# Optimization experiments

Measured on AMD Instinct MI355X. Metric: run time of the kernel, lower is better.

The kernel has to match this reference:

```python
import jax, jax.numpy as jnp
import numpy as np

K = 5          # top_k periods
KERNEL = 25    # moving-average kernel for series decomposition
D = 64         # d_model / channels
EPS = 1e-5     # BatchNorm eps (torch default)


def setup_inputs() -> dict:
    key = jax.random.key(0)
    k0, k1, k2, k3, k4 = jax.random.split(key, 5)
    B, T = 8, 2048
    x = jax.random.normal(k0, (B, T, D), jnp.float32)
    w1 = jax.random.normal(k1, (D, D, 3, 3), jnp.float32) * 0.05
    w2 = jax.random.normal(k2, (D, D, 3, 3), jnp.float32) * 0.05
    bn1_gamma = jnp.ones((D,), jnp.float32) + 0.1 * jax.random.normal(k3, (D,), jnp.float32)
    bn2_gamma = jnp.ones((D,), jnp.float32) + 0.1 * jax.random.normal(k4, (D,), jnp.float32)
    z = jnp.zeros((D,), jnp.float32)
    o = jnp.ones((D,), jnp.float32)
    return dict(x=x, w1=w1, w2=w2,
                bn1_gamma=bn1_gamma, bn1_beta=z, bn1_mean=z, bn1_var=o,
                bn2_gamma=bn2_gamma, bn2_beta=z, bn2_mean=z, bn2_var=o)


def _moving_avg(x, kernel):
    # AvgPool1d(stride=1, padding=(kernel-1)//2, count_include_pad=False) over time.
    T = x.shape[1]
    pad = (kernel - 1) // 2
    cs = jnp.concatenate([jnp.zeros_like(x[:, :1]), jnp.cumsum(x, axis=1)], axis=1)  # [B,T+1,C]
    t = jnp.arange(T)
    lo = jnp.clip(t - pad, 0, T)          # inclusive window start
    hi = jnp.clip(t + pad + 1, 0, T)      # exclusive window end
    sums = cs[:, hi] - cs[:, lo]
    return sums / (hi - lo).astype(x.dtype)[None, :, None]


def _auto_corr(s, k):
    T = s.shape[1]
    Xf = jnp.fft.rfft(s, axis=1)
    Pm = (Xf * jnp.conj(Xf)).real.mean(axis=-1)          # [B, T//2+1]
    r = jnp.fft.irfft(Pm, n=T, axis=1)                   # [B, T]
    r = r.at[:, 0].set(-jnp.inf)                          # forbid lag 0
    vals, idx = jax.lax.top_k(r, k)                       # [B,k]
    w = jax.nn.softmax(vals, axis=1)
    return idx, w


def _bn(z, gamma, beta, mean, var):
    return (z - mean) * (gamma * jax.lax.rsqrt(var + EPS)) + beta


def _process_one(s_b, p, w1, w2, bn1, bn2):
    # s_b: [T, C]; p: scalar int period.
    # Equivalent to: roll(s_b, -p), reflect-pad time to cyc*p, fold to [C,cyc,p],
    # Conv2dResBlock (3x3 zero-pad convs + eval BN + GELU + residual), unfold, crop to T.
    T, C = s_b.shape
    U = 2 * T - 2                               # static bound: cyc*p <= T+p-1 <= 2T-2
    u = jnp.arange(U)
    cyc = (T + p - 1) // p
    v = jnp.where(u < T, u, 2 * T - 2 - u)      # reflect extension index
    g = s_b[(v + p) % T]                         # [U,C] rolled-by-(-p) then reflect-padded
    r = u // p                                   # grid row (cycle)
    c = u % p                                    # grid col (phase)

    def conv3x3(z, w):
        # zero-padded 3x3 conv on the [cyc, p] grid, expressed on the flat time axis
        out = jnp.zeros_like(z)
        for dr in (-1, 0, 1):
            for dc in (-1, 0, 1):
                valid = (r + dr >= 0) & (r + dr < cyc) & (c + dc >= 0) & (c + dc < p)
                un = jnp.clip(u + dr * p + dc, 0, U - 1)
                zn = jnp.where(valid[:, None], z[un], 0.0)    # [U,C]
                out = out + zn @ w[:, :, dr + 1, dc + 1].T    # [U,Cout]
        return out

    h = _bn(conv3x3(g, w1), *bn1)
    h = jax.nn.gelu(h, approximate=False)
    h = _bn(conv3x3(h, w2), *bn2)
    return (g + h)[:T]                           # residual + unfold-crop


def reference(x, w1, w2, bn1_gamma, bn1_beta, bn1_mean, bn1_var,
              bn2_gamma, bn2_beta, bn2_mean, bn2_var):
    trend = _moving_avg(x, KERNEL)
    s = x - trend                                # seasonal
    idx, w = _auto_corr(s, K)                    # [B,K] periods, weights
    bn1 = (bn1_gamma, bn1_beta, bn1_mean, bn1_var)
    bn2 = (bn2_gamma, bn2_beta, bn2_mean, bn2_var)
    f = lambda sb, p: _process_one(sb, p, w1, w2, bn1, bn2)
    y = jax.vmap(lambda sb, pb: jax.vmap(lambda p: f(sb, p))(pb))(s, idx)  # [B,K,T,C]
    agg = jnp.einsum('bk,bktc->btc', w, y)
    return agg + trend + x
```

## Files before the change

### kernel.cpp

```cpp
#include <hip/hip_runtime.h>
#include <hip/hip_bf16.h>
#include <math.h>

#define TB 8
#define TT 2048
#define TD 64
#define TK 5
#define TPAD 12
#define EPSBN 1e-5f
#define UMAX 4096

#define ROWS 64
#define BAND 66
#define LROWS 198

#define ROWS2 16
#define BAND2 18
#define LROWS2 54
#define SH8   432
#define BUFB  6912

#define RSTR 272

typedef __attribute__((ext_vector_type(8))) short short8;
typedef __attribute__((ext_vector_type(4))) float f32x4;

#define OFF_S     0
#define OFF_SBF   1048576
#define OFF_R     1572864
#define OFF_IDX   1581056
#define OFF_W     1581096
#define OFF_WT1   1581136
#define OFF_WT2   1599568
#define OFF_H1    1618000

__global__ __launch_bounds__(256) void k_trend(const float* __restrict__ x,
                                               float* __restrict__ out, float* __restrict__ s,
                                               __hip_bfloat16* __restrict__ sbf,
                                               const float* __restrict__ w1, const float* __restrict__ w2,
                                               __hip_bfloat16* __restrict__ wt1, __hip_bfloat16* __restrict__ wt2,
                                               float* __restrict__ r)
{
    if (blockIdx.x >= 256) {
        int d = (blockIdx.x - 256) * 256 + threadIdx.x;
        if (d < TB * 1024) r[d] = 0.f;
        if (d < 36864) {
            int j = d & 7, l = (d >> 3) & 63, nt = (d >> 9) & 3, kb = d >> 11;
            int tap = kb >> 1, half = kb & 1;
            int co = nt * 16 + (l & 15);
            int ci = half * 32 + (l >> 4) * 8 + j;
            int src = (co * 64 + ci) * 9 + tap;
            wt1[d] = __float2bfloat16(w1[src]);
            wt2[d] = __float2bfloat16(w2[src]);
        }
        return;
    }
    int gid = blockIdx.x * 256 + threadIdx.x;
    int c = gid & 63;
    int tblk = (gid >> 6) & 127;
    int b = gid >> 13;
    int t0 = tblk * 16;
    const float* base = x + (size_t)b * TT * TD + c;
    float sum = 0.f;
    for (int tt = t0 - TPAD; tt <= t0 + TPAD; ++tt)
        if (tt >= 0 && tt < TT) sum += base[(size_t)tt * TD];
    size_t o = (size_t)b * TT * TD + (size_t)t0 * TD + c;
    #pragma unroll
    for (int i = 0; i < 16; ++i) {
        int t = t0 + i;
        int lo = t - TPAD; if (lo < 0) lo = 0;
        int hi = t + TPAD; if (hi > TT - 1) hi = TT - 1;
        float tr = sum / (float)(hi - lo + 1);
        float xv = base[(size_t)t * TD];
        out[o] = xv + tr;
        float sv = xv - tr;
        s[o] = sv;
        sbf[o] = __float2bfloat16(sv);
        int addt = t + TPAD + 1, subt = t - TPAD;
        if (addt < TT) sum += base[(size_t)addt * TD];
        if (subt >= 0) sum -= base[(size_t)subt * TD];
        o += TD;
    }
}

__global__ __launch_bounds__(256) void k_autocorr(const float* __restrict__ s, float* __restrict__ r)
{
    int id = blockIdx.x;
    int b = id & 7;
    int i0 = id >> 3;
    int l0 = (i0 & 63) * 16 + 1;
    int tq = i0 >> 6;
    const float* sb = s + (size_t)b * TT * TD;
    int cg = (threadIdx.x & 15) * 4;
    int tg = threadIdx.x >> 4;
    int t0 = tq * 512 + tg * 32;
    const int RB = TD * 4;
    const int TTB = TT * TD * 4;
    float acc[16];
    #pragma unroll
    for (int j = 0; j < 16; ++j) acc[j] = 0.f;
    float4 win[16];
    int wi = t0 + l0; if (wi >= TT) wi -= TT;
    int woff = wi * RB + cg * 4;
    int aoff = t0 * RB + cg * 4;
    #pragma unroll
    for (int m = 0; m < 16; ++m) {
        win[m] = *(const float4*)((const char*)sb + woff);
        woff += RB; if (woff >= TTB) woff -= TTB;
    }
    float4 a_pf = *(const float4*)((const char*)sb + aoff);
    aoff += RB;
    for (int it = 0; it < 2; ++it) {
        #pragma unroll
        for (int jj = 0; jj < 16; ++jj) {
            float4 a = a_pf;
            a_pf = *(const float4*)((const char*)sb + aoff);
            aoff += RB;
            #pragma unroll
            for (int j = 0; j < 16; ++j) {
                float4 w = win[(jj + j) & 15];
                acc[j] = fmaf(a.x, w.x, acc[j]);
                acc[j] = fmaf(a.y, w.y, acc[j]);
                acc[j] = fmaf(a.z, w.z, acc[j]);
                acc[j] = fmaf(a.w, w.w, acc[j]);
            }
            win[jj] = *(const float4*)((const char*)sb + woff);
            woff += RB; if (woff >= TTB) woff -= TTB;
        }
    }
    __shared__ float red[16 * RSTR];
    #pragma unroll
    for (int j = 0; j < 16; ++j) red[j * RSTR + threadIdx.x] = acc[j];
    __syncthreads();
    int j = threadIdx.x >> 4, i = threadIdx.x & 15;
    float v = 0.f;
    #pragma unroll
    for (int m = 0; m < 16; ++m) v += red[j * RSTR + i + 16 * m];
    #pragma unroll
    for (int mask = 8; mask; mask >>= 1) v += __shfl_xor(v, mask);
    if (i == 0) atomicAdd(&r[(size_t)b * 1024 + (l0 - 1 + j)], v * (1.0f / 64.0f));
}

__global__ __launch_bounds__(256) void k_topk(const float* __restrict__ r,
                                              int* __restrict__ selidx, float* __restrict__ selw)
{
    int b = blockIdx.x;
    __shared__ float v[1024];
    __shared__ float redv[256]; __shared__ int redi[256];
    __shared__ int s_idx[6]; __shared__ float s_val[6]; __shared__ int slots;
    for (int i = threadIdx.x; i < 1024; i += 256) v[i] = r[(size_t)b * 1024 + i];
    if (threadIdx.x == 0) slots = 0;
    __syncthreads();
    for (int round = 0; round < 5; ++round) {
        if (slots >= 5) break;
        float bv = -INFINITY; int bi = 1 << 30;
        for (int i = threadIdx.x; i < 1024; i += 256) {
            float val = v[i];
            if (val > bv) { bv = val; bi = i; }
        }
        redv[threadIdx.x] = bv; redi[threadIdx.x] = bi;
        __syncthreads();
        for (int off = 128; off; off >>= 1) {
            if (threadIdx.x < off) {
                float ov = redv[threadIdx.x + off]; int oi = redi[threadIdx.x + off];
                float mv = redv[threadIdx.x];       int mi = redi[threadIdx.x];
                if (ov > mv || (ov == mv && oi < mi)) { redv[threadIdx.x] = ov; redi[threadIdx.x] = oi; }
            }
            __syncthreads();
        }
        if (threadIdx.x == 0) {
            int lag = redi[0] + 1; float val = redv[0];
            s_idx[slots] = lag; s_val[slots] = val; slots++;
            if (slots < 5 && lag < 1024) { s_idx[slots] = 2048 - lag; s_val[slots] = val; slots++; }
            v[lag - 1] = -INFINITY;
        }
        __syncthreads();
    }
    if (threadIdx.x == 0) {
        float mx = -INFINITY;
        for (int i = 0; i < 5; ++i) mx = fmaxf(mx, s_val[i]);
        float e[5], sum = 0.f;
        for (int i = 0; i < 5; ++i) { e[i] = expf(s_val[i] - mx); sum += e[i]; }
        for (int i = 0; i < 5; ++i) { selidx[b * TK + i] = s_idx[i]; selw[b * TK + i] = e[i] / sum; }
    }
}

__global__ __launch_bounds__(256) void k_mm1(
    const short* __restrict__ s_bf, const short* __restrict__ wtp,
    const float* __restrict__ g1, const float* __restrict__ b1,
    const float* __restrict__ m1, const float* __restrict__ v1,
    const int* __restrict__ sel, __hip_bfloat16* __restrict__ h1)
{
    int b = blockIdx.z, k = blockIdx.y;
    int p = sel[b * TK + k];
    int cyc = (TT + p - 1) / p;
    int U = cyc * p;
    int u0 = blockIdx.x * ROWS;
    if (u0 >= U) return;
    __shared__ short As[LROWS * 64];

    const short* sb = s_bf + (size_t)b * TT * TD;
    for (int q = threadIdx.x; q < LROWS * 8; q += 256) {
        int row = q >> 3, ch = (q & 7) * 8;
        int band = row / BAND, i = row - band * BAND;
        int w = u0 + (band - 1) * p - 1 + i;
        int wc = min(max(w, 0), 2 * TT - 2);
        int v = (wc < TT) ? wc : (2 * TT - 2 - wc);
        int sr = (v + p) & (TT - 1);
        short8 d = *(const short8*)(sb + (size_t)sr * TD + ch);
        int off = (row * 128 + ch * 2) ^ ((row & 7) << 4);
        *(short8*)((char*)As + off) = d;
    }
    __syncthreads();

    int lane = threadIdx.x & 63;
    int wv = threadIdx.x >> 6;
    int lr = lane & 15;
    int kg = lane >> 4;
    int lu = wv * 16 + lr;
    int u = u0 + lu;
    bool inU = (u < U);
    int r = u / p, c = u - r * p;
    bool topf = (r == 0), botf = (r == cyc - 1), leftf = (c == 0), rightf = (c == p - 1);

    f32x4 acc[4] = {};
    short8 zero = {};
    #pragma unroll
    for (int kb = 0; kb < 18; ++kb) {
        const int tap = kb >> 1, half = kb & 1;
        const int dr = tap / 3 - 1, dc = tap % 3 - 1;
        int ldsrow = (dr + 1) * BAND + lu + 1 + dc;
        int off = (ldsrow * 128 + half * 64 + kg * 16) ^ ((ldsrow & 7) << 4);
        short8 a = *(const short8*)((const char*)As + off);
        bool valid = inU
                   && !(dr == -1 && topf) && !(dr == 1 && botf)
                   && !(dc == -1 && leftf) && !(dc == 1 && rightf);
        if (!valid) a = zero;
        #pragma unroll
        for (int nt = 0; nt < 4; ++nt) {
            short8 bq = *(const short8*)(wtp + (size_t)(kb * 4 + nt) * 512 + lane * 8);
            acc[nt] = __builtin_amdgcn_mfma_f32_16x16x32_bf16(a, bq, acc[nt], 0, 0, 0);
        }
    }
    __hip_bfloat16* ho = h1 + (size_t)(b * TK + k) * (UMAX * TD);
    #pragma unroll
    for (int nt = 0; nt < 4; ++nt) {
        int co = nt * 16 + lr;
        float scale = g1[co] * rsqrtf(v1[co] + EPSBN);
        float bias = b1[co] - m1[co] * scale;
        #pragma unroll
        for (int q = 0; q < 4; ++q) {
            int uo = u0 + wv * 16 + kg * 4 + q;
            if (uo < U) {
                float z = acc[nt][q] * scale + bias;
                float ge = 0.5f * z * (1.0f + erff(z * 0.70710678118654752f));
                ho[(size_t)uo * TD + co] = __float2bfloat16(ge);
            }
        }
    }
}

__global__ __launch_bounds__(256) void k_mm2f(
    const short* __restrict__ h1, const short* __restrict__ wtp,
    const float* __restrict__ s,
    const float* __restrict__ g2, const float* __restrict__ b2,
    const float* __restrict__ m2, const float* __restrict__ v2,
    const int* __restrict__ sel, const float* __restrict__ selw,
    float* __restrict__ out)
{
    int b = blockIdx.y;
    int u0 = blockIdx.x * ROWS2;
    int tid = threadIdx.x;
    __shared__ short As[2 * LROWS2 * 64];

    int lane = tid & 63, wv = tid >> 6, lr = lane & 15, kg = lane >> 4;
    int u = u0 + lr;
    const float* sb = s + (size_t)b * TT * TD;

    f32x4 accT = {};
    float gacc[4] = {0.f, 0.f, 0.f, 0.f};
    short8 sreg[2];
    short8 zero = {};

    {
        int p0 = sel[b * TK];
        const short* hb = h1 + (size_t)(b * TK) * (UMAX * TD);
        #pragma unroll
        for (int it = 0; it < 2; ++it) {
            int q = tid + it * 256;
            if (q < SH8) {
                int row = q >> 3, ch = (q & 7) * 8;
                int band = row / BAND2, i = row - band * BAND2;
                int w = u0 + (band - 1) * p0 - 1 + i;
                int wc = min(max(w, 0), UMAX - 1);
                short8 d = *(const short8*)(hb + (size_t)wc * TD + ch);
                int off = (row * 128 + ch * 2) ^ ((row & 7) << 4);
                *(short8*)((char*)As + off) = d;
            }
        }
    }
    __syncthreads();

    for (int k = 0; k < TK; ++k) {
        int p = sel[b * TK + k];
        float wk = selw[b * TK + k];
        int cyc = (TT + p - 1) / p;
        if (k < TK - 1) {
            int pn = sel[b * TK + k + 1];
            const short* hb = h1 + (size_t)(b * TK + k + 1) * (UMAX * TD);
            #pragma unroll
            for (int it = 0; it < 2; ++it) {
                int q = tid + it * 256;
                if (q < SH8) {
                    int row = q >> 3, ch = (q & 7) * 8;
                    int band = row / BAND2, i = row - band * BAND2;
                    int w = u0 + (band - 1) * pn - 1 + i;
                    int wc = min(max(w, 0), UMAX - 1);
                    sreg[it] = *(const short8*)(hb + (size_t)wc * TD + ch);
                }
            }
        }
        const char* Ab = (const char*)As + (k & 1) * BUFB;
        int r = u / p, c = u - r * p;
        bool topf = (r == 0), botf = (r == cyc - 1), leftf = (c == 0), rightf = (c == p - 1);
        f32x4 accP[2] = {};
        #pragma unroll
        for (int kb = 0; kb < 18; ++kb) {
            const int tap = kb >> 1, half = kb & 1;
            const int dr = tap / 3 - 1, dc = tap % 3 - 1;
            int ldsrow = (dr + 1) * BAND2 + lr + 1 + dc;
            int off = (ldsrow * 128 + half * 64 + kg * 16) ^ ((ldsrow & 7) << 4);
            short8 a = *(const short8*)(Ab + off);
            bool valid = !(dr == -1 && topf) && !(dr == 1 && botf)
                       && !(dc == -1 && leftf) && !(dc == 1 && rightf);
            if (!valid) a = zero;
            short8 bq = *(const short8*)(wtp + (size_t)(kb * 4 + wv) * 512 + lane * 8);
            accP[kb & 1] = __builtin_amdgcn_mfma_f32_16x16x32_bf16(a, bq, accP[kb & 1], 0, 0, 0);
        }
        #pragma unroll
        for (int e = 0; e < 4; ++e) accT[e] += wk * (accP[0][e] + accP[1][e]);
        #pragma unroll
        for (int q = 0; q < 4; ++q) {
            int uo = u0 + kg * 4 + q;
            int sr = (uo + p) & (TT - 1);
            gacc[q] = fmaf(wk, sb[(size_t)sr * TD + wv * 16 + lr], gacc[q]);
        }
        __syncthreads();
        if (k < TK - 1) {
            char* Aw = (char*)As + ((k + 1) & 1) * BUFB;
            #pragma unroll
            for (int it = 0; it < 2; ++it) {
                int q = tid + it * 256;
                if (q < SH8) {
                    int row = q >> 3, ch = (q & 7) * 8;
                    int off = (row * 128 + ch * 2) ^ ((row & 7) << 4);
                    *(short8*)(Aw + off) = sreg[it];
                }
            }
            __syncthreads();
        }
    }

    float* ob = out + (size_t)b * TT * TD;
    int co = wv * 16 + lr;
    float scale = g2[co] * rsqrtf(v2[co] + EPSBN);
    float bias = b2[co] - m2[co] * scale;
    #pragma unroll
    for (int q = 0; q < 4; ++q) {
        int uo = u0 + kg * 4 + q;
        size_t idx = (size_t)uo * TD + co;
        ob[idx] = ob[idx] + gacc[q] + scale * accT[q] + bias;
    }
}

extern "C" void kernel_launch(void* const* d_in, const int* in_sizes, int n_in,
                              void* d_out, int out_size, void* d_ws, size_t ws_size,
                              hipStream_t stream)
{
    const float* x  = (const float*)d_in[0];
    const float* w1 = (const float*)d_in[1];
    const float* w2 = (const float*)d_in[2];
    const float* g1 = (const float*)d_in[3];
    const float* b1 = (const float*)d_in[4];
    const float* m1 = (const float*)d_in[5];
    const float* v1 = (const float*)d_in[6];
    const float* g2 = (const float*)d_in[7];
    const float* b2 = (const float*)d_in[8];
    const float* m2 = (const float*)d_in[9];
    const float* v2 = (const float*)d_in[10];

    float* ws    = (float*)d_ws;
    float* s     = ws + OFF_S;
    __hip_bfloat16* sbf = (__hip_bfloat16*)(ws + OFF_SBF);
    float* r     = ws + OFF_R;
    int*   sel   = (int*)(ws + OFF_IDX);
    float* selw  = ws + OFF_W;
    __hip_bfloat16* wt1 = (__hip_bfloat16*)(ws + OFF_WT1);
    __hip_bfloat16* wt2 = (__hip_bfloat16*)(ws + OFF_WT2);
    __hip_bfloat16* h1  = (__hip_bfloat16*)(ws + OFF_H1);
    float* out   = (float*)d_out;

    k_trend   <<<dim3(400),         dim3(256), 0, stream>>>(x, out, s, sbf, w1, w2, wt1, wt2, r);
    k_autocorr<<<dim3(2048),        dim3(256), 0, stream>>>(s, r);
    k_topk    <<<dim3(TB),          dim3(256), 0, stream>>>(r, sel, selw);
    k_mm1     <<<dim3(64, TK, TB),  dim3(256), 0, stream>>>((const short*)sbf, (const short*)wt1,
                                                            g1, b1, m1, v1, sel, h1);
    k_mm2f    <<<dim3(128, TB),     dim3(256), 0, stream>>>((const short*)h1, (const short*)wt2, s,
                                                            g2, b2, m2, v2, sel, selw, out);
}
```

Baseline: 122.1 us.

## Stage autocorrelation tiles in LDS with 64x64 time-lag blocking

```diff
diff --git a/kernel.cpp b/kernel.cpp
--- a/kernel.cpp
+++ b/kernel.cpp
@@ -19,8 +19,6 @@
 #define LROWS2 54
 #define SH8   432
 #define BUFB  6912
-
-#define RSTR 272
 
 typedef __attribute__((ext_vector_type(8))) short short8;
 typedef __attribute__((ext_vector_type(4))) float f32x4;
@@ -88,57 +86,64 @@
     int id = blockIdx.x;
     int b = id & 7;
     int i0 = id >> 3;
-    int l0 = (i0 & 63) * 16 + 1;
-    int tq = i0 >> 6;
+    int tchunk = i0 & 31;
+    int lagblk = i0 >> 5;
+    int t0 = tchunk * 64;
+    int l0 = lagblk * 64 + 1;
     const float* sb = s + (size_t)b * TT * TD;
+    __shared__ float A[64 * 64];
+    __shared__ float W[127 * 64];
+
+    #pragma unroll
+    for (int it = 0; it < 4; ++it) {
+        int q = threadIdx.x + it * 256;
+        int row = q >> 4, f4 = (q & 15) * 4;
+        *(float4*)(A + row * 64 + f4) = *(const float4*)(sb + (size_t)(t0 + row) * TD + f4);
+    }
+    for (int q = threadIdx.x; q < 127 * 16; q += 256) {
+        int row = q >> 4, f4 = (q & 15) * 4;
+        int gr = t0 + l0 + row; if (gr >= TT) gr -= TT;
+        *(float4*)(W + row * 64 + f4) = *(const float4*)(sb + (size_t)gr * TD + f4);
+    }
+    __syncthreads();
+
     int cg = (threadIdx.x & 15) * 4;
-    int tg = threadIdx.x >> 4;
-    int t0 = tq * 512 + tg * 32;
-    const int RB = TD * 4;
-    const int TTB = TT * TD * 4;
+    int slot = threadIdx.x >> 4;
+    int lsub = slot >> 2;
+    int ts = slot & 3;
+    int abase = ts * 16;
+    int wbase = ts * 16 + lsub * 16;
+
     float acc[16];
     #pragma unroll
     for (int j = 0; j < 16; ++j) acc[j] = 0.f;
     float4 win[16];
-    int wi = t0 + l0; if (wi >= TT) wi -= TT;
-    int woff = wi * RB + cg * 4;
-    int aoff = t0 * RB + cg * 4;
-    #pragma unroll
-    for (int m = 0; m < 16; ++m) {
-        win[m] = *(const float4*)((const char*)sb + woff);
-        woff += RB; if (woff >= TTB) woff -= TTB;
-    }
-    float4 a_pf = *(const float4*)((const char*)sb + aoff);
-    aoff += RB;
-    for (int it = 0; it < 2; ++it) {
-        #pragma unroll
-        for (int jj = 0; jj < 16; ++jj) {
-            float4 a = a_pf;
-            a_pf = *(const float4*)((const char*)sb + aoff);
-            aoff += RB;
-            #pragma unroll
-            for (int j = 0; j < 16; ++j) {
-                float4 w = win[(jj + j) & 15];
-                acc[j] = fmaf(a.x, w.x, acc[j]);
-                acc[j] = fmaf(a.y, w.y, acc[j]);
-                acc[j] = fmaf(a.z, w.z, acc[j]);
-                acc[j] = fmaf(a.w, w.w, acc[j]);
-            }
-            win[jj] = *(const float4*)((const char*)sb + woff);
-            woff += RB; if (woff >= TTB) woff -= TTB;
-        }
-    }
-    __shared__ float red[16 * RSTR];
-    #pragma unroll
-    for (int j = 0; j < 16; ++j) red[j * RSTR + threadIdx.x] = acc[j];
-    __syncthreads();
-    int j = threadIdx.x >> 4, i = threadIdx.x & 15;
-    float v = 0.f;
-    #pragma unroll
-    for (int m = 0; m < 16; ++m) v += red[j * RSTR + i + 16 * m];
-    #pragma unroll
-    for (int mask = 8; mask; mask >>= 1) v += __shfl_xor(v, mask);
-    if (i == 0) atomicAdd(&r[(size_t)b * 1024 + (l0 - 1 + j)], v * (1.0f / 64.0f));
+    #pragma unroll
+    for (int m = 0; m < 16; ++m) win[m] = *(const float4*)(W + (wbase + m) * 64 + cg);
+
+    #pragma unroll
+    for (int step = 0; step < 16; ++step) {
+        float4 a = *(const float4*)(A + (abase + step) * 64 + cg);
+        #pragma unroll
+        for (int j = 0; j < 16; ++j) {
+            float4 w = win[(step + j) & 15];
+            acc[j] = fmaf(a.x, w.x, acc[j]);
+            acc[j] = fmaf(a.y, w.y, acc[j]);
+            acc[j] = fmaf(a.z, w.z, acc[j]);
+            acc[j] = fmaf(a.w, w.w, acc[j]);
+        }
+        if (step < 15) win[step & 15] = *(const float4*)(W + (wbase + step + 16) * 64 + cg);
+    }
+
+    int lane = threadIdx.x & 63;
+    #pragma unroll
+    for (int j = 0; j < 16; ++j) {
+        float v = acc[j];
+        #pragma unroll
+        for (int mask = 32; mask; mask >>= 1) v += __shfl_xor(v, mask);
+        if (lane == 0)
+            atomicAdd(&r[(size_t)b * 1024 + (l0 - 1 + lsub * 16 + j)], v * (1.0f / 64.0f));
+    }
 }
 
 __global__ __launch_bounds__(256) void k_topk(const float* __restrict__ r,
@@ -401,7 +406,7 @@
     float* out   = (float*)d_out;
 
     k_trend   <<<dim3(400),         dim3(256), 0, stream>>>(x, out, s, sbf, w1, w2, wt1, wt2, r);
-    k_autocorr<<<dim3(2048),        dim3(256), 0, stream>>>(s, r);
+    k_autocorr<<<dim3(4096),        dim3(256), 0, stream>>>(s, r);
     k_topk    <<<dim3(TB),          dim3(256), 0, stream>>>(r, sel, selw);
     k_mm1     <<<dim3(64, TK, TB),  dim3(256), 0, stream>>>((const short*)sbf, (const short*)wt1,
                                                             g1, b1, m1, v1, sel, h1);
```

Result: slower. 219.4 us (+79.8%).

## Compute autocorrelation with bf16 MFMA and rescore top candidates in fp32

Applied to the files above, without the earlier changes.

```diff
diff --git a/kernel.cpp b/kernel.cpp
--- a/kernel.cpp
+++ b/kernel.cpp
@@ -20,7 +20,7 @@
 #define SH8   432
 #define BUFB  6912
 
-#define RSTR 272
+#define ACG 17
 
 typedef __attribute__((ext_vector_type(8))) short short8;
 typedef __attribute__((ext_vector_type(4))) float f32x4;
@@ -33,6 +33,7 @@
 #define OFF_WT1   1581136
 #define OFF_WT2   1599568
 #define OFF_H1    1618000
+#define OFF_CAND  6860880
 
 __global__ __launch_bounds__(256) void k_trend(const float* __restrict__ x,
                                                float* __restrict__ out, float* __restrict__ s,
@@ -83,76 +84,91 @@
     }
 }
 
-__global__ __launch_bounds__(256) void k_autocorr(const float* __restrict__ s, float* __restrict__ r)
+__global__ __launch_bounds__(256) void k_ac_mfma(const short* __restrict__ sbf16, float* __restrict__ r)
 {
     int id = blockIdx.x;
     int b = id & 7;
-    int i0 = id >> 3;
-    int l0 = (i0 & 63) * 16 + 1;
-    int tq = i0 >> 6;
-    const float* sb = s + (size_t)b * TT * TD;
-    int cg = (threadIdx.x & 15) * 4;
-    int tg = threadIdx.x >> 4;
-    int t0 = tq * 512 + tg * 32;
-    const int RB = TD * 4;
-    const int TTB = TT * TD * 4;
-    float acc[16];
-    #pragma unroll
-    for (int j = 0; j < 16; ++j) acc[j] = 0.f;
-    float4 win[16];
-    int wi = t0 + l0; if (wi >= TT) wi -= TT;
-    int woff = wi * RB + cg * 4;
-    int aoff = t0 * RB + cg * 4;
-    #pragma unroll
-    for (int m = 0; m < 16; ++m) {
-        win[m] = *(const float4*)((const char*)sb + woff);
-        woff += RB; if (woff >= TTB) woff -= TTB;
-    }
-    float4 a_pf = *(const float4*)((const char*)sb + aoff);
-    aoff += RB;
-    for (int it = 0; it < 2; ++it) {
-        #pragma unroll
-        for (int jj = 0; jj < 16; ++jj) {
-            float4 a = a_pf;
-            a_pf = *(const float4*)((const char*)sb + aoff);
-            aoff += RB;
-            #pragma unroll
-            for (int j = 0; j < 16; ++j) {
-                float4 w = win[(jj + j) & 15];
-                acc[j] = fmaf(a.x, w.x, acc[j]);
-                acc[j] = fmaf(a.y, w.y, acc[j]);
-                acc[j] = fmaf(a.z, w.z, acc[j]);
-                acc[j] = fmaf(a.w, w.w, acc[j]);
-            }
-            win[jj] = *(const float4*)((const char*)sb + woff);
-            woff += RB; if (woff >= TTB) woff -= TTB;
-        }
-    }
-    __shared__ float red[16 * RSTR];
-    #pragma unroll
-    for (int j = 0; j < 16; ++j) red[j * RSTR + threadIdx.x] = acc[j];
-    __syncthreads();
-    int j = threadIdx.x >> 4, i = threadIdx.x & 15;
-    float v = 0.f;
-    #pragma unroll
-    for (int m = 0; m < 16; ++m) v += red[j * RSTR + i + 16 * m];
-    #pragma unroll
-    for (int mask = 8; mask; mask >>= 1) v += __shfl_xor(v, mask);
-    if (i == 0) atomicAdd(&r[(size_t)b * 1024 + (l0 - 1 + j)], v * (1.0f / 64.0f));
-}
-
-__global__ __launch_bounds__(256) void k_topk(const float* __restrict__ r,
-                                              int* __restrict__ selidx, float* __restrict__ selw)
+    int slot = id >> 3;
+    int g = slot % ACG;
+    int qq = slot / ACG;
+    int d0 = g * 4;
+    int t0 = qq * 32;
+    const short* sb = sbf16 + (size_t)b * TT * TD;
+
+    __shared__ short Atile[2][1024];
+    __shared__ short Btile[6][1024];
+    __shared__ float scr[4][16 * 17];
+
+    int tid = threadIdx.x;
+    if (tid < 128) {
+        int dst = (tid * 16) ^ (((tid >> 3) & 7) << 4);
+        *(short8*)((char*)Atile[t0 & 1] + dst) =
+            *(const short8*)(sb + (size_t)((t0 & 127) * 1024) + tid * 8);
+        #pragma unroll
+        for (int j = 0; j < 4; ++j) {
+            int xi = t0 + d0 + j;
+            *(short8*)((char*)Btile[xi % 6] + dst) =
+                *(const short8*)(sb + (size_t)((xi & 127) * 1024) + tid * 8);
+        }
+    }
+    __syncthreads();
+
+    int lane = tid & 63, wv = tid >> 6;
+    int fr = lane & 15, kg = lane >> 4;
+    int roff0 = (fr * 128 + kg * 16) ^ ((fr & 7) << 4);
+    int roff1 = roff0 ^ 64;
+    int myD = d0 + wv;
+
+    f32x4 acc = {};
+    for (int stp = 0; stp < 32; ++stp) {
+        int ti = t0 + stp;
+        short8 sA, sB;
+        if (tid < 128) {
+            sA = *(const short8*)(sb + (size_t)(((ti + 1) & 127) * 1024) + tid * 8);
+            sB = *(const short8*)(sb + (size_t)(((ti + d0 + 4) & 127) * 1024) + tid * 8);
+        }
+        const char* Ab = (const char*)Atile[ti & 1];
+        const char* Bb = (const char*)Btile[(ti + myD) % 6];
+        short8 a0 = *(const short8*)(Ab + roff0);
+        short8 a1 = *(const short8*)(Ab + roff1);
+        short8 b0 = *(const short8*)(Bb + roff0);
+        short8 b1 = *(const short8*)(Bb + roff1);
+        acc = __builtin_amdgcn_mfma_f32_16x16x32_bf16(a0, b0, acc, 0, 0, 0);
+        acc = __builtin_amdgcn_mfma_f32_16x16x32_bf16(a1, b1, acc, 0, 0, 0);
+        if (tid < 128) {
+            int dst = (tid * 16) ^ (((tid >> 3) & 7) << 4);
+            *(short8*)((char*)Atile[(ti + 1) & 1] + dst) = sA;
+            *(short8*)((char*)Btile[(ti + d0 + 4) % 6] + dst) = sB;
+        }
+        __syncthreads();
+    }
+
+    float* sc = scr[wv];
+    #pragma unroll
+    for (int q = 0; q < 4; ++q)
+        sc[(kg * 4 + q) * 17 + fr] = acc[q];
+    __syncthreads();
+    if (lane < 31) {
+        int d = lane - 15;
+        int lag = 16 * myD + d;
+        if (lag >= 1 && lag <= 1024) {
+            int m0 = d < 0 ? -d : 0;
+            int m1 = d < 0 ? 16 : 16 - d;
+            float v = 0.f;
+            for (int m = m0; m < m1; ++m) v += sc[m * 17 + m + d];
+            atomicAdd(&r[(size_t)b * 1024 + (lag - 1)], v * (1.0f / 64.0f));
+        }
+    }
+}
+
+__global__ __launch_bounds__(256) void k_cand(const float* __restrict__ r, int* __restrict__ cand)
 {
     int b = blockIdx.x;
     __shared__ float v[1024];
     __shared__ float redv[256]; __shared__ int redi[256];
-    __shared__ int s_idx[6]; __shared__ float s_val[6]; __shared__ int slots;
     for (int i = threadIdx.x; i < 1024; i += 256) v[i] = r[(size_t)b * 1024 + i];
-    if (threadIdx.x == 0) slots = 0;
-    __syncthreads();
-    for (int round = 0; round < 5; ++round) {
-        if (slots >= 5) break;
+    __syncthreads();
+    for (int round = 0; round < 8; ++round) {
         float bv = -INFINITY; int bi = 1 << 30;
         for (int i = threadIdx.x; i < 1024; i += 256) {
             float val = v[i];
@@ -169,14 +185,52 @@
             __syncthreads();
         }
         if (threadIdx.x == 0) {
-            int lag = redi[0] + 1; float val = redv[0];
-            s_idx[slots] = lag; s_val[slots] = val; slots++;
-            if (slots < 5 && lag < 1024) { s_idx[slots] = 2048 - lag; s_val[slots] = val; slots++; }
+            int lag = redi[0] + 1;
+            cand[b * 8 + round] = lag;
             v[lag - 1] = -INFINITY;
         }
         __syncthreads();
     }
+}
+
+__global__ __launch_bounds__(512) void k_rescore5(const float* __restrict__ s, const int* __restrict__ cand,
+                                                  int* __restrict__ selidx, float* __restrict__ selw)
+{
+    int b = blockIdx.x;
+    int wv = threadIdx.x >> 6, lane = threadIdx.x & 63;
+    const float* sb = s + (size_t)b * TT * TD;
+    int lag = cand[b * 8 + wv];
+    int cg = (lane & 15) * 4;
+    int t0 = (lane >> 4) * 512;
+    float acc = 0.f;
+    #pragma unroll 8
+    for (int t = t0; t < t0 + 512; ++t) {
+        const float4 a = *(const float4*)(sb + ((size_t)t << 6) + cg);
+        const float4 w = *(const float4*)(sb + ((size_t)((t + lag) & (TT - 1)) << 6) + cg);
+        acc = fmaf(a.x, w.x, acc);
+        acc = fmaf(a.y, w.y, acc);
+        acc = fmaf(a.z, w.z, acc);
+        acc = fmaf(a.w, w.w, acc);
+    }
+    #pragma unroll
+    for (int mask = 32; mask; mask >>= 1) acc += __shfl_xor(acc, mask);
+    __shared__ float vals[8];
+    if (lane == 0) vals[wv] = acc * (1.0f / 64.0f);
+    __syncthreads();
     if (threadIdx.x == 0) {
+        float vv[8]; int ll[8]; bool used[8];
+        #pragma unroll
+        for (int i = 0; i < 8; ++i) { vv[i] = vals[i]; ll[i] = cand[b * 8 + i]; used[i] = false; }
+        int s_idx[6]; float s_val[6]; int slots = 0;
+        while (slots < 5) {
+            float bv = -INFINITY; int bi = -1;
+            for (int i = 0; i < 8; ++i) {
+                if (!used[i] && (vv[i] > bv || (vv[i] == bv && ll[i] < ll[bi]))) { bv = vv[i]; bi = i; }
+            }
+            used[bi] = true;
+            s_idx[slots] = ll[bi]; s_val[slots] = bv; slots++;
+            if (slots < 5 && ll[bi] < 1024) { s_idx[slots] = 2048 - ll[bi]; s_val[slots] = bv; slots++; }
+        }
         float mx = -INFINITY;
         for (int i = 0; i < 5; ++i) mx = fmaxf(mx, s_val[i]);
         float e[5], sum = 0.f;
@@ -398,11 +452,13 @@
     __hip_bfloat16* wt1 = (__hip_bfloat16*)(ws + OFF_WT1);
     __hip_bfloat16* wt2 = (__hip_bfloat16*)(ws + OFF_WT2);
     __hip_bfloat16* h1  = (__hip_bfloat16*)(ws + OFF_H1);
+    int*   cand  = (int*)(ws + OFF_CAND);
     float* out   = (float*)d_out;
 
     k_trend   <<<dim3(400),         dim3(256), 0, stream>>>(x, out, s, sbf, w1, w2, wt1, wt2, r);
-    k_autocorr<<<dim3(2048),        dim3(256), 0, stream>>>(s, r);
-    k_topk    <<<dim3(TB),          dim3(256), 0, stream>>>(r, sel, selw);
+    k_ac_mfma <<<dim3(544),         dim3(256), 0, stream>>>((const short*)sbf, r);
+    k_cand    <<<dim3(TB),          dim3(256), 0, stream>>>(r, cand);
+    k_rescore5<<<dim3(TB),          dim3(512), 0, stream>>>(s, cand, sel, selw);
     k_mm1     <<<dim3(64, TK, TB),  dim3(256), 0, stream>>>((const short*)sbf, (const short*)wt1,
                                                             g1, b1, m1, v1, sel, h1);
     k_mm2f    <<<dim3(128, TB),     dim3(256), 0, stream>>>((const short*)h1, (const short*)wt2, s,
```

Measured after the change: 164.2 us. 1.34x slower.
